# Optimization experiments

Measured on AMD Instinct MI355X. Metric: run time of the kernel, lower is better.

## Reference

```python
import jax, jax.numpy as jnp
import numpy as np

B = 8      # number of drug-target pairs in the packed batch
NR = 3200  # total packed residues
NA = 320   # total packed atoms
TD = 512   # target (GearNet) feature dim
DD = 128   # drug (EGNN) feature dim
H = 128    # hidden_dim


def setup_inputs() -> dict:
    key = jax.random.key(0)
    ks = jax.random.split(key, 10)
    seg_res = jnp.sort(jax.random.randint(ks[0], (NR,), 0, B, dtype=jnp.int32))
    seg_atom = jnp.sort(jax.random.randint(ks[1], (NA,), 0, B, dtype=jnp.int32))
    return {
        "target_feature": jax.random.normal(ks[2], (NR, TD), jnp.float32),
        "drug_feature": jax.random.normal(ks[3], (NA, DD), jnp.float32),
        "target_pos": jax.random.normal(ks[4], (NR, 3), jnp.float32) * 10.0,
        "drug_pos": jax.random.normal(ks[5], (NA, 3), jnp.float32) * 10.0,
        "Wt": jax.random.normal(ks[6], (TD, H), jnp.float32) / np.sqrt(TD).astype(np.float32),
        "bt": jnp.zeros((H,), jnp.float32),
        "Wd": jax.random.normal(ks[7], (DD, H), jnp.float32) / np.sqrt(DD).astype(np.float32),
        "bd": jnp.zeros((H,), jnp.float32),
        "seg_res": seg_res,
        "seg_atom": seg_atom,
    }


def reference(target_feature, drug_feature, target_pos, drug_pos, Wt, bt, Wd, bd, seg_res, seg_atom):
    # Linear projections (torchdrug MLP with a single hidden dim == plain Linear)
    tf = target_feature @ Wt + bt  # [NR, H]
    df = drug_feature @ Wd + bd    # [NA, H]

    # Block-diagonal mask: pair (i, j) is valid iff residue i and atom j belong
    # to the same DT-pair (replaces the Python loop that zeroes cross blocks).
    mask = seg_res[:, None] == seg_atom[None, :]  # [NR, NA]

    # Pairwise residue-atom distances
    D = jnp.linalg.norm(target_pos[:, None, :] - drug_pos[None, :, :], axis=-1)  # [NR, NA]

    # Per-block min/max distance (min/max over the masked block only)
    row_min = jnp.min(jnp.where(mask, D, jnp.inf), axis=1)   # [NR]
    row_max = jnp.max(jnp.where(mask, D, -jnp.inf), axis=1)  # [NR]
    dmin = jax.ops.segment_min(row_min, seg_res, num_segments=B)  # [B]
    dmax = jax.ops.segment_max(row_max, seg_res, num_segments=B)  # [B]
    dmin = jnp.where(jnp.isfinite(dmin), dmin, 0.0)
    dmax = jnp.where(jnp.isfinite(dmax), dmax, 1.0)
    denom = jnp.where(dmax > dmin, dmax - dmin, 1.0)

    # Normalized distance inside blocks, zero outside (matches the torch loop)
    dnorm = jnp.where(mask, (D - dmin[seg_res][:, None]) / denom[seg_res][:, None], 0.0)

    # Feature difference inside blocks, zero outside
    imap = jnp.where(mask[:, :, None], tf[:, None, :] - df[None, :, :], 0.0)  # [NR, NA, H]

    # scaled=False -> no 1/sqrt(hidden_dim) scaling
    return jnp.tanh(imap + dnorm[:, :, None])
```

## Files before the change

kernel.cpp:

```cpp
#include <hip/hip_runtime.h>
#include <math.h>

constexpr int NR = 3200;
constexpr int NA = 320;
constexpr int TD = 512;
constexpr int DD = 128;
constexpr int H  = 128;
constexpr int B  = 8;
constexpr int NP = NR * NA;
constexpr long long TOTAL = (long long)NP * H;

__global__ void init_minmax(int* dmin_bits, int* dmax_bits) {
    int t = threadIdx.x;
    if (t < B) {
        dmin_bits[t] = 0x7F800000;
        dmax_bits[t] = (int)0xFF800000;
    }
}

template<int K, int ROWS>
__global__ void gemm_rows(const float* __restrict__ A,
                          const float* __restrict__ W,
                          const float* __restrict__ bias,
                          float* __restrict__ out) {
    __shared__ float sA[ROWS * K];
    const int i0 = blockIdx.x * ROWS;
    const int h  = threadIdx.x;

    for (int idx = h; idx < ROWS * K; idx += H)
        sA[idx] = A[(long long)i0 * K + idx];
    __syncthreads();

    float acc[ROWS];
    const float bv = bias[h];
#pragma unroll
    for (int r = 0; r < ROWS; r++) acc[r] = bv;

#pragma unroll 4
    for (int k = 0; k < K; k++) {
        const float w = W[k * H + h];
#pragma unroll
        for (int r = 0; r < ROWS; r++)
            acc[r] = fmaf(sA[r * K + k], w, acc[r]);
    }
#pragma unroll
    for (int r = 0; r < ROWS; r++)
        out[(i0 + r) * H + h] = acc[r];
}

__global__ void dist_kernel(const float* __restrict__ tpos,
                            const float* __restrict__ dpos,
                            const int* __restrict__ seg_res,
                            const int* __restrict__ seg_atom,
                            float* __restrict__ Dbuf,
                            int* dmin_bits, int* dmax_bits) {
    const int i = blockIdx.x;
    const int j = threadIdx.x;
    const int sr = seg_res[i];

    const float tx = tpos[i * 3 + 0];
    const float ty = tpos[i * 3 + 1];
    const float tz = tpos[i * 3 + 2];
    const float dx = tx - dpos[j * 3 + 0];
    const float dy = ty - dpos[j * 3 + 1];
    const float dz = tz - dpos[j * 3 + 2];
    const float d  = sqrtf(dx * dx + dy * dy + dz * dz);
    Dbuf[i * NA + j] = d;

    const bool m = (sr == seg_atom[j]);
    float vmin = m ? d :  INFINITY;
    float vmax = m ? d : -INFINITY;
#pragma unroll
    for (int off = 32; off > 0; off >>= 1) {
        vmin = fminf(vmin, __shfl_down(vmin, off));
        vmax = fmaxf(vmax, __shfl_down(vmax, off));
    }
    __shared__ float smin[5], smax[5];
    const int wid  = j >> 6;
    const int lane = j & 63;
    if (lane == 0) { smin[wid] = vmin; smax[wid] = vmax; }
    __syncthreads();
    if (j == 0) {
        float mn = smin[0], mx = smax[0];
#pragma unroll
        for (int w = 1; w < 5; w++) { mn = fminf(mn, smin[w]); mx = fmaxf(mx, smax[w]); }
        if (mn < INFINITY)  atomicMin(&dmin_bits[sr], __float_as_int(mn));
        if (mx > -INFINITY) atomicMax(&dmax_bits[sr], __float_as_int(mx));
    }
}

__global__ void dnorm_kernel(float* __restrict__ Dbuf,
                             const int* __restrict__ seg_res,
                             const int* __restrict__ seg_atom,
                             const int* __restrict__ dmin_bits,
                             const int* __restrict__ dmax_bits) {
    const int p = blockIdx.x * blockDim.x + threadIdx.x;
    if (p >= NP) return;
    const int i = p / NA;
    const int j = p - i * NA;
    float outv = -1.0f;
    const int sr = seg_res[i];
    if (sr == seg_atom[j]) {
        const int mnb = dmin_bits[sr];
        const int mxb = dmax_bits[sr];
        const float dmin = (mnb == 0x7F800000) ? 0.0f : __int_as_float(mnb);
        const float dmax = (mxb == (int)0xFF800000) ? 1.0f : __int_as_float(mxb);
        const float denom = (dmax > dmin) ? (dmax - dmin) : 1.0f;
        outv = (Dbuf[p] - dmin) / denom;
    }
    Dbuf[p] = outv;
}

__device__ __forceinline__ float fast_tanh(float x) {
    const float cx = fminf(fmaxf(x, -15.0f), 15.0f);
    const float e  = __expf(2.0f * cx);
    return 1.0f - __fdividef(2.0f, e + 1.0f);
}

__global__ void final_kernel(const float* __restrict__ tf,
                             const float* __restrict__ df,
                             const float* __restrict__ dnorm,
                             float* __restrict__ out) {
    const long long t    = (long long)blockIdx.x * blockDim.x + threadIdx.x;
    const long long base = t * 4;
    if (base >= TOTAL) return;
    const int p = (int)(base >> 7);
    const int h = (int)(base & 127);
    const float dn = dnorm[p];
    float4 o;
    if (dn >= 0.0f) {
        const int i = p / NA;
        const int j = p - i * NA;
        const float4 tv = *(const float4*)(tf + i * H + h);
        const float4 dv = *(const float4*)(df + j * H + h);
        o.x = fast_tanh(tv.x - dv.x + dn);
        o.y = fast_tanh(tv.y - dv.y + dn);
        o.z = fast_tanh(tv.z - dv.z + dn);
        o.w = fast_tanh(tv.w - dv.w + dn);
    } else {
        o.x = 0.0f; o.y = 0.0f; o.z = 0.0f; o.w = 0.0f;
    }
    *(float4*)(out + base) = o;
}

extern "C" void kernel_launch(void* const* d_in, const int* in_sizes, int n_in,
                              void* d_out, int out_size, void* d_ws, size_t ws_size,
                              hipStream_t stream) {
    const float* target_feature = (const float*)d_in[0];
    const float* drug_feature   = (const float*)d_in[1];
    const float* target_pos     = (const float*)d_in[2];
    const float* drug_pos       = (const float*)d_in[3];
    const float* Wt             = (const float*)d_in[4];
    const float* bt             = (const float*)d_in[5];
    const float* Wd             = (const float*)d_in[6];
    const float* bd             = (const float*)d_in[7];
    const int*   seg_res        = (const int*)d_in[8];
    const int*   seg_atom       = (const int*)d_in[9];
    float* out = (float*)d_out;

    float* ws   = (float*)d_ws;
    float* tf   = ws;
    float* df   = tf + NR * H;
    float* Dbuf = df + NA * H;
    int*   dmin_bits = (int*)(Dbuf + NP);
    int*   dmax_bits = dmin_bits + B;

    init_minmax<<<1, 64, 0, stream>>>(dmin_bits, dmax_bits);
    gemm_rows<TD, 4><<<NR / 4, H, 0, stream>>>(target_feature, Wt, bt, tf);
    gemm_rows<DD, 4><<<NA / 4, H, 0, stream>>>(drug_feature, Wd, bd, df);
    dist_kernel<<<NR, NA, 0, stream>>>(target_pos, drug_pos, seg_res, seg_atom,
                                       Dbuf, dmin_bits, dmax_bits);
    dnorm_kernel<<<(NP + 255) / 256, 256, 0, stream>>>(Dbuf, seg_res, seg_atom,
                                                       dmin_bits, dmax_bits);
    final_kernel<<<(int)(TOTAL / 4 / 256), 256, 0, stream>>>(tf, df, Dbuf, out);
}
```

Baseline: 671.2 us.

## Fuse dnorm normalization into final kernel and split GEMM K across halves

Removes the separate pass that read and rewrote the full distance buffer. The final kernel now computes the mask and normalized distance itself, using per-segment (dmin, 1/denom) values from a tiny finalize kernel. The min/max init moves into the first GEMM launch, and each GEMM block uses 256 threads that split K in half and combine the halves through shared memory. Output stores become nontemporal, trading an extra index/mask computation per element in the big kernel for one less full-size memory pass.

Result: faster. 632.8 us (-5.7%).

```diff
diff --git a/kernel.cpp b/kernel.cpp
--- a/kernel.cpp
+++ b/kernel.cpp
@@ -10,42 +10,55 @@
 constexpr int NP = NR * NA;
 constexpr long long TOTAL = (long long)NP * H;
 
-__global__ void init_minmax(int* dmin_bits, int* dmax_bits) {
-    int t = threadIdx.x;
-    if (t < B) {
+typedef float f4 __attribute__((ext_vector_type(4)));
+
+template<int K, int ROWS>
+__global__ __launch_bounds__(256) void gemm_rows(const float* __restrict__ A,
+                                                 const float* __restrict__ W,
+                                                 const float* __restrict__ bias,
+                                                 float* __restrict__ out,
+                                                 int* dmin_bits, int* dmax_bits) {
+    __shared__ float sA[ROWS * K];
+    __shared__ float sAcc[ROWS * H];
+    const int t    = threadIdx.x;
+    const int h    = t & (H - 1);
+    const int half = t >> 7;
+    const int i0   = blockIdx.x * ROWS;
+
+    if (dmin_bits != nullptr && blockIdx.x == 0 && t < B) {
         dmin_bits[t] = 0x7F800000;
         dmax_bits[t] = (int)0xFF800000;
     }
-}
 
-template<int K, int ROWS>
-__global__ void gemm_rows(const float* __restrict__ A,
-                          const float* __restrict__ W,
-                          const float* __restrict__ bias,
-                          float* __restrict__ out) {
-    __shared__ float sA[ROWS * K];
-    const int i0 = blockIdx.x * ROWS;
-    const int h  = threadIdx.x;
-
-    for (int idx = h; idx < ROWS * K; idx += H)
-        sA[idx] = A[(long long)i0 * K + idx];
+    for (int idx = t; idx < ROWS * K; idx += 256)
+        sA[idx] = A[i0 * K + idx];
     __syncthreads();
 
     float acc[ROWS];
-    const float bv = bias[h];
 #pragma unroll
-    for (int r = 0; r < ROWS; r++) acc[r] = bv;
+    for (int r = 0; r < ROWS; r++) acc[r] = 0.0f;
 
+    const int k0 = half * (K / 2);
+    const int k1 = k0 + (K / 2);
 #pragma unroll 4
-    for (int k = 0; k < K; k++) {
+    for (int k = k0; k < k1; k++) {
         const float w = W[k * H + h];
 #pragma unroll
         for (int r = 0; r < ROWS; r++)
             acc[r] = fmaf(sA[r * K + k], w, acc[r]);
     }
+
+    if (half == 1) {
 #pragma unroll
-    for (int r = 0; r < ROWS; r++)
-        out[(i0 + r) * H + h] = acc[r];
+        for (int r = 0; r < ROWS; r++) sAcc[r * H + h] = acc[r];
+    }
+    __syncthreads();
+    if (half == 0) {
+        const float bv = bias[h];
+#pragma unroll
+        for (int r = 0; r < ROWS; r++)
+            out[(i0 + r) * H + h] = acc[r] + sAcc[r * H + h] + bv;
+    }
 }
 
 __global__ void dist_kernel(const float* __restrict__ tpos,
@@ -89,26 +102,18 @@
     }
 }
 
-__global__ void dnorm_kernel(float* __restrict__ Dbuf,
-                             const int* __restrict__ seg_res,
-                             const int* __restrict__ seg_atom,
-                             const int* __restrict__ dmin_bits,
-                             const int* __restrict__ dmax_bits) {
-    const int p = blockIdx.x * blockDim.x + threadIdx.x;
-    if (p >= NP) return;
-    const int i = p / NA;
-    const int j = p - i * NA;
-    float outv = -1.0f;
-    const int sr = seg_res[i];
-    if (sr == seg_atom[j]) {
-        const int mnb = dmin_bits[sr];
-        const int mxb = dmax_bits[sr];
+__global__ void finalize_params(const int* __restrict__ dmin_bits,
+                                const int* __restrict__ dmax_bits,
+                                float2* __restrict__ params) {
+    const int s = threadIdx.x;
+    if (s < B) {
+        const int mnb = dmin_bits[s];
+        const int mxb = dmax_bits[s];
         const float dmin = (mnb == 0x7F800000) ? 0.0f : __int_as_float(mnb);
         const float dmax = (mxb == (int)0xFF800000) ? 1.0f : __int_as_float(mxb);
         const float denom = (dmax > dmin) ? (dmax - dmin) : 1.0f;
-        outv = (Dbuf[p] - dmin) / denom;
+        params[s] = make_float2(dmin, 1.0f / denom);
     }
-    Dbuf[p] = outv;
 }
 
 __device__ __forceinline__ float fast_tanh(float x) {
@@ -117,30 +122,33 @@
     return 1.0f - __fdividef(2.0f, e + 1.0f);
 }
 
-__global__ void final_kernel(const float* __restrict__ tf,
-                             const float* __restrict__ df,
-                             const float* __restrict__ dnorm,
-                             float* __restrict__ out) {
-    const long long t    = (long long)blockIdx.x * blockDim.x + threadIdx.x;
-    const long long base = t * 4;
-    if (base >= TOTAL) return;
-    const int p = (int)(base >> 7);
-    const int h = (int)(base & 127);
-    const float dn = dnorm[p];
-    float4 o;
-    if (dn >= 0.0f) {
-        const int i = p / NA;
-        const int j = p - i * NA;
-        const float4 tv = *(const float4*)(tf + i * H + h);
-        const float4 dv = *(const float4*)(df + j * H + h);
+__global__ __launch_bounds__(256) void final_kernel(const float* __restrict__ tf,
+                                                    const float* __restrict__ df,
+                                                    const float* __restrict__ Dbuf,
+                                                    const int* __restrict__ seg_res,
+                                                    const int* __restrict__ seg_atom,
+                                                    const float2* __restrict__ params,
+                                                    float* __restrict__ out) {
+    const int t    = blockIdx.x * 256 + threadIdx.x;
+    const int base = t << 2;
+    const int p    = base >> 7;
+    const int h    = base & 127;
+    const int i    = p / NA;
+    const int j    = p - i * NA;
+
+    f4 o = {0.0f, 0.0f, 0.0f, 0.0f};
+    const int sr = seg_res[i];
+    if (sr == seg_atom[j]) {
+        const float2 pp = params[sr];
+        const float  dn = (Dbuf[p] - pp.x) * pp.y;
+        const f4 tv = *(const f4*)(tf + i * H + h);
+        const f4 dv = *(const f4*)(df + j * H + h);
         o.x = fast_tanh(tv.x - dv.x + dn);
         o.y = fast_tanh(tv.y - dv.y + dn);
         o.z = fast_tanh(tv.z - dv.z + dn);
         o.w = fast_tanh(tv.w - dv.w + dn);
-    } else {
-        o.x = 0.0f; o.y = 0.0f; o.z = 0.0f; o.w = 0.0f;
     }
-    *(float4*)(out + base) = o;
+    __builtin_nontemporal_store(o, (f4*)(out + base));
 }
 
 extern "C" void kernel_launch(void* const* d_in, const int* in_sizes, int n_in,
@@ -162,15 +170,17 @@
     float* tf   = ws;
     float* df   = tf + NR * H;
     float* Dbuf = df + NA * H;
-    int*   dmin_bits = (int*)(Dbuf + NP);
-    int*   dmax_bits = dmin_bits + B;
+    int*    dmin_bits = (int*)(Dbuf + NP);
+    int*    dmax_bits = dmin_bits + B;
+    float2* params    = (float2*)(dmax_bits + B);
 
-    init_minmax<<<1, 64, 0, stream>>>(dmin_bits, dmax_bits);
-    gemm_rows<TD, 4><<<NR / 4, H, 0, stream>>>(target_feature, Wt, bt, tf);
-    gemm_rows<DD, 4><<<NA / 4, H, 0, stream>>>(drug_feature, Wd, bd, df);
+    gemm_rows<TD, 4><<<NR / 4, 256, 0, stream>>>(target_feature, Wt, bt, tf,
+                                                 dmin_bits, dmax_bits);
+    gemm_rows<DD, 4><<<NA / 4, 256, 0, stream>>>(drug_feature, Wd, bd, df,
+                                                 nullptr, nullptr);
     dist_kernel<<<NR, NA, 0, stream>>>(target_pos, drug_pos, seg_res, seg_atom,
                                        Dbuf, dmin_bits, dmax_bits);
-    dnorm_kernel<<<(NP + 255) / 256, 256, 0, stream>>>(Dbuf, seg_res, seg_atom,
-                                                       dmin_bits, dmax_bits);
-    final_kernel<<<(int)(TOTAL / 4 / 256), 256, 0, stream>>>(tf, df, Dbuf, out);
+    finalize_params<<<1, 64, 0, stream>>>(dmin_bits, dmax_bits, params);
+    final_kernel<<<(int)(TOTAL / 4 / 256), 256, 0, stream>>>(tf, df, Dbuf, seg_res,
+                                                             seg_atom, params, out);
 }
```

## Fuse projections and min/max into one kernel, recompute distances in output kernel

Applied to the files above, without the earlier changes.

The two GEMM projections and the per-row min/max distance reduction now run as branches of a single launch, with each GEMM's K dimension split across two halves of a 256-thread block. The stored distance buffer and the separate normalization pass are gone; the output kernel recomputes each residue-atom distance and normalizes it inline. The output kernel writes 8 floats per thread with nontemporal stores on a 2D grid. This removes two kernel launches and the round trip of a 4 MB intermediate buffer, at the cost of recomputing sqrt per output pair and some shared-memory reduction overhead.

Result: slower. 743.9 us (+10.8%).

```diff
diff --git a/kernel.cpp b/kernel.cpp
--- a/kernel.cpp
+++ b/kernel.cpp
@@ -7,108 +7,122 @@
 constexpr int DD = 128;
 constexpr int H  = 128;
 constexpr int B  = 8;
-constexpr int NP = NR * NA;
-constexpr long long TOTAL = (long long)NP * H;
-
-__global__ void init_minmax(int* dmin_bits, int* dmax_bits) {
-    int t = threadIdx.x;
+
+constexpr int ROWS_T  = 4;
+constexpr int ROWS_D  = 8;
+constexpr int NBLK_T  = NR / ROWS_T;
+constexpr int NBLK_D  = NA / ROWS_D;
+constexpr int NBLK_MM = NR;
+
+typedef float f4 __attribute__((ext_vector_type(4)));
+
+__global__ void init_minmax(int* cells) {
+    const int t = threadIdx.x;
     if (t < B) {
-        dmin_bits[t] = 0x7F800000;
-        dmax_bits[t] = (int)0xFF800000;
+        cells[t]     = 0x7F800000;
+        cells[B + t] = (int)0xFF800000;
     }
 }
 
-template<int K, int ROWS>
-__global__ void gemm_rows(const float* __restrict__ A,
-                          const float* __restrict__ W,
-                          const float* __restrict__ bias,
-                          float* __restrict__ out) {
-    __shared__ float sA[ROWS * K];
-    const int i0 = blockIdx.x * ROWS;
-    const int h  = threadIdx.x;
-
-    for (int idx = h; idx < ROWS * K; idx += H)
-        sA[idx] = A[(long long)i0 * K + idx];
-    __syncthreads();
-
-    float acc[ROWS];
-    const float bv = bias[h];
-#pragma unroll
-    for (int r = 0; r < ROWS; r++) acc[r] = bv;
-
+__global__ __launch_bounds__(256) void mega_kernel(
+    const float* __restrict__ At, const float* __restrict__ Wt, const float* __restrict__ bt,
+    const float* __restrict__ Ad, const float* __restrict__ Wd, const float* __restrict__ bd,
+    const float* __restrict__ tpos, const float* __restrict__ dpos,
+    const int* __restrict__ seg_res, const int* __restrict__ seg_atom,
+    float* __restrict__ tf, float* __restrict__ df, int* __restrict__ cells) {
+    __shared__ float sA[ROWS_T * TD];
+    __shared__ float sAcc[ROWS_D * H];
+    const int b = blockIdx.x;
+    const int t = threadIdx.x;
+
+    if (b < NBLK_T) {
+        const int h = t & (H - 1), half = t >> 7, i0 = b * ROWS_T;
+        for (int idx = t; idx < ROWS_T * TD; idx += 256)
+            sA[idx] = At[i0 * TD + idx];
+        __syncthreads();
+        float acc[ROWS_T];
+#pragma unroll
+        for (int r = 0; r < ROWS_T; r++) acc[r] = 0.0f;
+        const int k0 = half * (TD / 2), k1 = k0 + (TD / 2);
 #pragma unroll 4
-    for (int k = 0; k < K; k++) {
-        const float w = W[k * H + h];
-#pragma unroll
-        for (int r = 0; r < ROWS; r++)
-            acc[r] = fmaf(sA[r * K + k], w, acc[r]);
+        for (int k = k0; k < k1; k++) {
+            const float w = Wt[k * H + h];
+#pragma unroll
+            for (int r = 0; r < ROWS_T; r++)
+                acc[r] = fmaf(sA[r * TD + k], w, acc[r]);
+        }
+        if (half) {
+#pragma unroll
+            for (int r = 0; r < ROWS_T; r++) sAcc[r * H + h] = acc[r];
+        }
+        __syncthreads();
+        if (!half) {
+            const float bv = bt[h];
+#pragma unroll
+            for (int r = 0; r < ROWS_T; r++)
+                tf[(i0 + r) * H + h] = acc[r] + sAcc[r * H + h] + bv;
+        }
+    } else if (b < NBLK_T + NBLK_D) {
+        const int h = t & (H - 1), half = t >> 7, i0 = (b - NBLK_T) * ROWS_D;
+        for (int idx = t; idx < ROWS_D * DD; idx += 256)
+            sA[idx] = Ad[i0 * DD + idx];
+        __syncthreads();
+        float acc[ROWS_D];
+#pragma unroll
+        for (int r = 0; r < ROWS_D; r++) acc[r] = 0.0f;
+        const int k0 = half * (DD / 2), k1 = k0 + (DD / 2);
+#pragma unroll 4
+        for (int k = k0; k < k1; k++) {
+            const float w = Wd[k * H + h];
+#pragma unroll
+            for (int r = 0; r < ROWS_D; r++)
+                acc[r] = fmaf(sA[r * DD + k], w, acc[r]);
+        }
+        if (half) {
+#pragma unroll
+            for (int r = 0; r < ROWS_D; r++) sAcc[r * H + h] = acc[r];
+        }
+        __syncthreads();
+        if (!half) {
+            const float bv = bd[h];
+#pragma unroll
+            for (int r = 0; r < ROWS_D; r++)
+                df[(i0 + r) * H + h] = acc[r] + sAcc[r * H + h] + bv;
+        }
+    } else {
+        const int i  = b - NBLK_T - NBLK_D;
+        const int sr = seg_res[i];
+        const float tx = tpos[3 * i], ty = tpos[3 * i + 1], tz = tpos[3 * i + 2];
+        float vmin = INFINITY, vmax = -INFINITY;
+        for (int j = t; j < NA; j += 256) {
+            if (seg_atom[j] == sr) {
+                const float dx = tx - dpos[3 * j];
+                const float dy = ty - dpos[3 * j + 1];
+                const float dz = tz - dpos[3 * j + 2];
+                const float d  = sqrtf(dx * dx + dy * dy + dz * dz);
+                vmin = fminf(vmin, d);
+                vmax = fmaxf(vmax, d);
+            }
+        }
+#pragma unroll
+        for (int off = 32; off > 0; off >>= 1) {
+            vmin = fminf(vmin, __shfl_down(vmin, off));
+            vmax = fmaxf(vmax, __shfl_down(vmax, off));
+        }
+        const int wid = t >> 6, lane = t & 63;
+        if (lane == 0) { sAcc[wid] = vmin; sAcc[4 + wid] = vmax; }
+        __syncthreads();
+        if (t == 0) {
+            float mn = sAcc[0], mx = sAcc[4];
+#pragma unroll
+            for (int w = 1; w < 4; w++) {
+                mn = fminf(mn, sAcc[w]);
+                mx = fmaxf(mx, sAcc[4 + w]);
+            }
+            if (mn < INFINITY)  atomicMin(&cells[sr],     __float_as_int(mn));
+            if (mx > -INFINITY) atomicMax(&cells[B + sr], __float_as_int(mx));
+        }
     }
-#pragma unroll
-    for (int r = 0; r < ROWS; r++)
-        out[(i0 + r) * H + h] = acc[r];
-}
-
-__global__ void dist_kernel(const float* __restrict__ tpos,
-                            const float* __restrict__ dpos,
-                            const int* __restrict__ seg_res,
-                            const int* __restrict__ seg_atom,
-                            float* __restrict__ Dbuf,
-                            int* dmin_bits, int* dmax_bits) {
-    const int i = blockIdx.x;
-    const int j = threadIdx.x;
-    const int sr = seg_res[i];
-
-    const float tx = tpos[i * 3 + 0];
-    const float ty = tpos[i * 3 + 1];
-    const float tz = tpos[i * 3 + 2];
-    const float dx = tx - dpos[j * 3 + 0];
-    const float dy = ty - dpos[j * 3 + 1];
-    const float dz = tz - dpos[j * 3 + 2];
-    const float d  = sqrtf(dx * dx + dy * dy + dz * dz);
-    Dbuf[i * NA + j] = d;
-
-    const bool m = (sr == seg_atom[j]);
-    float vmin = m ? d :  INFINITY;
-    float vmax = m ? d : -INFINITY;
-#pragma unroll
-    for (int off = 32; off > 0; off >>= 1) {
-        vmin = fminf(vmin, __shfl_down(vmin, off));
-        vmax = fmaxf(vmax, __shfl_down(vmax, off));
-    }
-    __shared__ float smin[5], smax[5];
-    const int wid  = j >> 6;
-    const int lane = j & 63;
-    if (lane == 0) { smin[wid] = vmin; smax[wid] = vmax; }
-    __syncthreads();
-    if (j == 0) {
-        float mn = smin[0], mx = smax[0];
-#pragma unroll
-        for (int w = 1; w < 5; w++) { mn = fminf(mn, smin[w]); mx = fmaxf(mx, smax[w]); }
-        if (mn < INFINITY)  atomicMin(&dmin_bits[sr], __float_as_int(mn));
-        if (mx > -INFINITY) atomicMax(&dmax_bits[sr], __float_as_int(mx));
-    }
-}
-
-__global__ void dnorm_kernel(float* __restrict__ Dbuf,
-                             const int* __restrict__ seg_res,
-                             const int* __restrict__ seg_atom,
-                             const int* __restrict__ dmin_bits,
-                             const int* __restrict__ dmax_bits) {
-    const int p = blockIdx.x * blockDim.x + threadIdx.x;
-    if (p >= NP) return;
-    const int i = p / NA;
-    const int j = p - i * NA;
-    float outv = -1.0f;
-    const int sr = seg_res[i];
-    if (sr == seg_atom[j]) {
-        const int mnb = dmin_bits[sr];
-        const int mxb = dmax_bits[sr];
-        const float dmin = (mnb == 0x7F800000) ? 0.0f : __int_as_float(mnb);
-        const float dmax = (mxb == (int)0xFF800000) ? 1.0f : __int_as_float(mxb);
-        const float denom = (dmax > dmin) ? (dmax - dmin) : 1.0f;
-        outv = (Dbuf[p] - dmin) / denom;
-    }
-    Dbuf[p] = outv;
 }
 
 __device__ __forceinline__ float fast_tanh(float x) {
@@ -117,30 +131,45 @@
     return 1.0f - __fdividef(2.0f, e + 1.0f);
 }
 
-__global__ void final_kernel(const float* __restrict__ tf,
-                             const float* __restrict__ df,
-                             const float* __restrict__ dnorm,
-                             float* __restrict__ out) {
-    const long long t    = (long long)blockIdx.x * blockDim.x + threadIdx.x;
-    const long long base = t * 4;
-    if (base >= TOTAL) return;
-    const int p = (int)(base >> 7);
-    const int h = (int)(base & 127);
-    const float dn = dnorm[p];
-    float4 o;
-    if (dn >= 0.0f) {
-        const int i = p / NA;
-        const int j = p - i * NA;
-        const float4 tv = *(const float4*)(tf + i * H + h);
-        const float4 dv = *(const float4*)(df + j * H + h);
-        o.x = fast_tanh(tv.x - dv.x + dn);
-        o.y = fast_tanh(tv.y - dv.y + dn);
-        o.z = fast_tanh(tv.z - dv.z + dn);
-        o.w = fast_tanh(tv.w - dv.w + dn);
-    } else {
-        o.x = 0.0f; o.y = 0.0f; o.z = 0.0f; o.w = 0.0f;
+__global__ __launch_bounds__(256) void final_kernel(
+    const float* __restrict__ tf, const float* __restrict__ df,
+    const float* __restrict__ tpos, const float* __restrict__ dpos,
+    const int* __restrict__ seg_res, const int* __restrict__ seg_atom,
+    const int* __restrict__ cells, float* __restrict__ out) {
+    const int i = blockIdx.y;
+    const int e = (blockIdx.x * 256 + threadIdx.x) * 8;
+    const int j = e >> 7;
+    const int h = e & 127;
+
+    f4 o0 = {0.0f, 0.0f, 0.0f, 0.0f};
+    f4 o1 = {0.0f, 0.0f, 0.0f, 0.0f};
+    const int sr = seg_res[i];
+    if (seg_atom[j] == sr) {
+        const int mnb = cells[sr];
+        const int mxb = cells[B + sr];
+        const float dmin = (mnb == 0x7F800000) ? 0.0f : __int_as_float(mnb);
+        const float dmax = (mxb == (int)0xFF800000) ? 1.0f : __int_as_float(mxb);
+        const float inv  = 1.0f / ((dmax > dmin) ? (dmax - dmin) : 1.0f);
+        const float dx = tpos[3 * i]     - dpos[3 * j];
+        const float dy = tpos[3 * i + 1] - dpos[3 * j + 1];
+        const float dz = tpos[3 * i + 2] - dpos[3 * j + 2];
+        const float dn = (sqrtf(dx * dx + dy * dy + dz * dz) - dmin) * inv;
+        const f4 tv0 = *(const f4*)(tf + i * H + h);
+        const f4 tv1 = *(const f4*)(tf + i * H + h + 4);
+        const f4 dv0 = *(const f4*)(df + j * H + h);
+        const f4 dv1 = *(const f4*)(df + j * H + h + 4);
+        o0.x = fast_tanh(tv0.x - dv0.x + dn);
+        o0.y = fast_tanh(tv0.y - dv0.y + dn);
+        o0.z = fast_tanh(tv0.z - dv0.z + dn);
+        o0.w = fast_tanh(tv0.w - dv0.w + dn);
+        o1.x = fast_tanh(tv1.x - dv1.x + dn);
+        o1.y = fast_tanh(tv1.y - dv1.y + dn);
+        o1.z = fast_tanh(tv1.z - dv1.z + dn);
+        o1.w = fast_tanh(tv1.w - dv1.w + dn);
     }
-    *(float4*)(out + base) = o;
+    float* dst = out + (long long)i * (NA * H) + e;
+    __builtin_nontemporal_store(o0, (f4*)dst);
+    __builtin_nontemporal_store(o1, (f4*)(dst + 4));
 }
 
 extern "C" void kernel_launch(void* const* d_in, const int* in_sizes, int n_in,
@@ -158,19 +187,15 @@
     const int*   seg_atom       = (const int*)d_in[9];
     float* out = (float*)d_out;
 
-    float* ws   = (float*)d_ws;
-    float* tf   = ws;
-    float* df   = tf + NR * H;
-    float* Dbuf = df + NA * H;
-    int*   dmin_bits = (int*)(Dbuf + NP);
-    int*   dmax_bits = dmin_bits + B;
-
-    init_minmax<<<1, 64, 0, stream>>>(dmin_bits, dmax_bits);
-    gemm_rows<TD, 4><<<NR / 4, H, 0, stream>>>(target_feature, Wt, bt, tf);
-    gemm_rows<DD, 4><<<NA / 4, H, 0, stream>>>(drug_feature, Wd, bd, df);
-    dist_kernel<<<NR, NA, 0, stream>>>(target_pos, drug_pos, seg_res, seg_atom,
-                                       Dbuf, dmin_bits, dmax_bits);
-    dnorm_kernel<<<(NP + 255) / 256, 256, 0, stream>>>(Dbuf, seg_res, seg_atom,
-                                                       dmin_bits, dmax_bits);
-    final_kernel<<<(int)(TOTAL / 4 / 256), 256, 0, stream>>>(tf, df, Dbuf, out);
-}
+    float* ws = (float*)d_ws;
+    float* tf = ws;
+    float* df = tf + NR * H;
+    int*   cells = (int*)(df + NA * H);
+
+    init_minmax<<<1, 64, 0, stream>>>(cells);
+    mega_kernel<<<NBLK_T + NBLK_D + NBLK_MM, 256, 0, stream>>>(
+        target_feature, Wt, bt, drug_feature, Wd, bd,
+        target_pos, drug_pos, seg_res, seg_atom, tf, df, cells);
+    final_kernel<<<dim3(NA * H / (8 * 256), NR), 256, 0, stream>>>(
+        tf, df, target_pos, drug_pos, seg_res, seg_atom, cells, out);
+}
```
